# Performance work log

Hardware: AMD Instinct MI355X
Metric: run time of the kernel (lower is better)

## Reference

```python
import jax, jax.numpy as jnp
import numpy as np

DIM = 1024
INTER = 1408
N_EXPERTS = 16
TOPK = 2
N_SHARED = 2
SHARED_INTER = N_SHARED * INTER
ROUTE_SCALE = 1.0


def setup_inputs() -> dict:
    key = jax.random.key(0)
    ks = jax.random.split(key, 16)
    s = 0.02
    return {
        "x": jax.random.normal(ks[0], (2, 2048, DIM), dtype=jnp.float32),
        "gate_w": jax.random.normal(ks[1], (DIM, N_EXPERTS), dtype=jnp.float32) * s,
        "gate_b": jnp.zeros((N_EXPERTS,), dtype=jnp.float32),
        "w1": jax.random.normal(ks[2], (N_EXPERTS, DIM, INTER), dtype=jnp.float32) * s,
        "b1": jnp.zeros((N_EXPERTS, INTER), dtype=jnp.float32),
        "w3": jax.random.normal(ks[3], (N_EXPERTS, DIM, INTER), dtype=jnp.float32) * s,
        "b3": jnp.zeros((N_EXPERTS, INTER), dtype=jnp.float32),
        "w2": jax.random.normal(ks[4], (N_EXPERTS, INTER, DIM), dtype=jnp.float32) * s,
        "b2": jnp.zeros((N_EXPERTS, DIM), dtype=jnp.float32),
        "sw1": jax.random.normal(ks[5], (DIM, SHARED_INTER), dtype=jnp.float32) * s,
        "sb1": jax.random.normal(ks[6], (SHARED_INTER,), dtype=jnp.float32) * s,
        "sw3": jax.random.normal(ks[7], (DIM, SHARED_INTER), dtype=jnp.float32) * s,
        "sb3": jax.random.normal(ks[8], (SHARED_INTER,), dtype=jnp.float32) * s,
        "sw2": jax.random.normal(ks[9], (SHARED_INTER, DIM), dtype=jnp.float32) * s,
        "sb2": jax.random.normal(ks[10], (DIM,), dtype=jnp.float32) * s,
    }


def reference(x, gate_w, gate_b, w1, b1, w3, b3, w2, b2, sw1, sb1, sw3, sb3, sw2, sb2):
    shape = x.shape
    xf = x.reshape(-1, DIM)  # [T, D]

    # Gate: softmax scores in fp32, top-k routing
    logits = xf @ gate_w + gate_b  # [T, E]
    scores = jax.nn.softmax(logits.astype(jnp.float32), axis=-1)
    top_vals, top_idx = jax.lax.top_k(scores, TOPK)  # [T, K]
    weights = (top_vals * ROUTE_SCALE).astype(x.dtype)

    # Combine weights per expert: [T, E]; zero for unselected experts
    cw = (jax.nn.one_hot(top_idx, N_EXPERTS, dtype=x.dtype) * weights[..., None]).sum(axis=1)

    # Routed experts (dense-per-expert SwiGLU, masked by combine weights)
    h = jnp.einsum('td,edh->teh', xf, w1) + b1  # [T, E, I]
    g = jnp.einsum('td,edh->teh', xf, w3) + b3
    a = jax.nn.silu(h) * g
    y = jnp.einsum('teh,ehd,te->td', a, w2, cw) + cw @ b2  # [T, D]

    # Shared expert SwiGLU
    z = (jax.nn.silu(xf @ sw1 + sb1) * (xf @ sw3 + sb3)) @ sw2 + sb2

    return (y + z).reshape(shape)
```

## Files before the change

kernel.cpp:

```cpp
#include <hip/hip_runtime.h>
#include <cstdint>
#include <cstddef>

#define T_TOKENS 4096
#define DIM      1024
#define INTER    1408
#define NEXP     16
#define SINTER   2816

typedef uint32_t u32;
typedef uint16_t u16;

using s8v = __attribute__((ext_vector_type(8))) short;
using f4v = __attribute__((ext_vector_type(4))) float;

__device__ __forceinline__ u16 f2bf(float f) {
  u32 u = __float_as_uint(f);
  return (u16)((u + 0x7fffu + ((u >> 16) & 1u)) >> 16);
}
__device__ __forceinline__ u32 pack2(float a, float b) {
  return (u32)f2bf(a) | ((u32)f2bf(b) << 16);
}

__device__ __forceinline__ void load_lds16(const u16* g, u16* l) {
  __builtin_amdgcn_global_load_lds((const __attribute__((address_space(1))) void*)g,
                                   (__attribute__((address_space(3))) void*)l,
                                   16, 0, 0);
}

__global__ __launch_bounds__(256)
void cvt_x(const float* __restrict__ in, u16* __restrict__ out) {
  const int i = (blockIdx.x * 256 + threadIdx.x) * 8;
  float4 a = *(const float4*)(in + i);
  float4 b = *(const float4*)(in + i + 4);
  uint4 o;
  o.x = pack2(a.x, a.y); o.y = pack2(a.z, a.w);
  o.z = pack2(b.x, b.y); o.w = pack2(b.z, b.w);
  *(uint4*)(out + i) = o;
}

__global__ __launch_bounds__(256)
void transpose_cvt(const float* __restrict__ in, u16* __restrict__ out,
                   int K, int N) {
  const size_t eoff = (size_t)blockIdx.z * K * N;
  const int n0 = blockIdx.x * 64, k0 = blockIdx.y * 64;
  __shared__ u16 t[64][72];

  const int tid = threadIdx.x;
  {
    const int r = tid >> 4, c4 = (tid & 15) * 4;
    const float* src = in + eoff + (size_t)k0 * N + n0;
#pragma unroll
    for (int i = 0; i < 4; i++) {
      int row = r + i * 16;
      float4 v = *(const float4*)(src + (size_t)row * N + c4);
      t[c4 + 0][row] = f2bf(v.x);
      t[c4 + 1][row] = f2bf(v.y);
      t[c4 + 2][row] = f2bf(v.z);
      t[c4 + 3][row] = f2bf(v.w);
    }
  }
  __syncthreads();
  {
    const int r = tid >> 3, cc = (tid & 7) * 8;
    u16* dst = out + eoff + (size_t)n0 * K + k0;
#pragma unroll
    for (int i = 0; i < 2; i++) {
      int row = r + i * 32;
      uint4 v = *(const uint4*)&t[row][cc];
      *(uint4*)(dst + (size_t)row * K + cc) = v;
    }
  }
}

__global__ __launch_bounds__(256)
void gate_kernel(const float* __restrict__ x, const float* __restrict__ gw,
                 const float* __restrict__ gb, int* __restrict__ counts,
                 int* __restrict__ g_e, int* __restrict__ g_r, float* __restrict__ g_w)
{
  const int tok  = blockIdx.x * 4 + (threadIdx.x >> 6);
  const int lane = threadIdx.x & 63;
  const float* xr = x + (size_t)tok * DIM;

  float acc[NEXP];
#pragma unroll
  for (int e = 0; e < NEXP; e++) acc[e] = 0.f;

  for (int k = lane; k < DIM; k += 64) {
    float xv = xr[k];
    const float* gwr = gw + k * NEXP;
#pragma unroll
    for (int e = 0; e < NEXP; e++) acc[e] = fmaf(xv, gwr[e], acc[e]);
  }
#pragma unroll
  for (int e = 0; e < NEXP; e++) {
    float v = acc[e];
#pragma unroll
    for (int off = 32; off > 0; off >>= 1) v += __shfl_xor(v, off, 64);
    acc[e] = v + gb[e];
  }
  if (lane == 0) {
    float mx = acc[0];
#pragma unroll
    for (int e = 1; e < NEXP; e++) mx = fmaxf(mx, acc[e]);
    float p[NEXP]; float s = 0.f;
#pragma unroll
    for (int e = 0; e < NEXP; e++) { p[e] = expf(acc[e] - mx); s += p[e]; }
    float inv = 1.f / s;
    int i0 = -1, i1 = -1; float v0 = -1e30f, v1 = -1e30f;
#pragma unroll
    for (int e = 0; e < NEXP; e++) {
      float pe = p[e] * inv;
      if (pe > v0)      { v1 = v0; i1 = i0; v0 = pe; i0 = e; }
      else if (pe > v1) { v1 = pe; i1 = e; }
    }
    int r0 = atomicAdd(&counts[i0], 1);
    int r1 = atomicAdd(&counts[i1], 1);
    g_e[tok * 2 + 0] = i0;  g_e[tok * 2 + 1] = i1;
    g_r[tok * 2 + 0] = r0;  g_r[tok * 2 + 1] = r1;
    g_w[tok * 2 + 0] = v0;  g_w[tok * 2 + 1] = v1;
  }
}

__global__ void scan_kernel(const int* __restrict__ counts, int* __restrict__ offsets) {
  if (threadIdx.x == 0) {
    int s = 0;
#pragma unroll
    for (int e = 0; e < NEXP; e++) { offsets[e] = s; s += counts[e]; }
    offsets[NEXP] = s;
  }
}

__global__ __launch_bounds__(256)
void scatter_kernel(const int* __restrict__ g_e, const int* __restrict__ g_r,
                    const float* __restrict__ g_w, const int* __restrict__ offsets,
                    int* __restrict__ tok_slot, float* __restrict__ w_slot)
{
  int t = blockIdx.x * blockDim.x + threadIdx.x;
  if (t >= T_TOKENS) return;
#pragma unroll
  for (int k = 0; k < 2; k++) {
    int e = g_e[t * 2 + k];
    int slot = offsets[e] + g_r[t * 2 + k];
    tok_slot[slot] = t;
    w_slot[slot] = g_w[t * 2 + k];
  }
}

template<bool GATHER>
__global__ __launch_bounds__(256, 2)
void ffn_up2(const u16* __restrict__ xbf,
             const u16* __restrict__ w1t, const float* __restrict__ b1p,
             const u16* __restrict__ w3t, const float* __restrict__ b3p,
             int N,
             const int* __restrict__ offsets, const int* __restrict__ tok_slot,
             u16* __restrict__ act)
{
  int e = 0, rowbase = 0, count = T_TOKENS;
  if constexpr (GATHER) {
    e = blockIdx.z; rowbase = offsets[e]; count = offsets[e + 1] - rowbase;
  }
  const int m0 = blockIdx.y * 128;
  if (m0 >= count) return;
  const int n0 = blockIdx.x * 128;

  const u16* W1 = w1t + (size_t)e * N * DIM;
  const u16* W3 = w3t + (size_t)e * N * DIM;
  const float* B1 = b1p + (size_t)e * N;
  const float* B3 = b3p + (size_t)e * N;

  __shared__ u16 sA[128 * 32];
  __shared__ u16 sB1[128 * 32];
  __shared__ u16 sB3[128 * 32];

  const int tid = threadIdx.x;
  const int lane = tid & 63;
  const int w = tid >> 6;

  const int kc8 = (lane & 3) * 8;
  const u16* aptr[2]; const u16* b1ptr[2]; const u16* b3ptr[2];
  u16 *ldsA[2], *ldsB1[2], *ldsB3[2];
#pragma unroll
  for (int i = 0; i < 2; i++) {
    const int row = i * 64 + w * 16 + (lane >> 2);
    const int ldoff = i * 2048 + w * 512 + lane * 8;
    ldsA[i] = sA + ldoff; ldsB1[i] = sB1 + ldoff; ldsB3[i] = sB3 + ldoff;
    int arow = m0 + row; if (arow > count - 1) arow = count - 1;
    const int tok = GATHER ? tok_slot[rowbase + arow] : arow;
    aptr[i]  = xbf + (size_t)tok * DIM + kc8;
    const int brow = n0 + row;
    b1ptr[i] = W1 + (size_t)brow * DIM + kc8;
    b3ptr[i] = W3 + (size_t)brow * DIM + kc8;
  }

  const int ln = lane & 15, q = lane >> 4;
  const int wm = (w & 1) * 64, wn = (w >> 1) * 64;
  const u16* pa  = sA  + (wm + ln) * 32 + q * 8;
  const u16* pb1 = sB1 + (wn + ln) * 32 + q * 8;
  const u16* pb3 = sB3 + (wn + ln) * 32 + q * 8;

  f4v acc1[4][4] = {};
  f4v acc3[4][4] = {};

  for (int k0 = 0; k0 < DIM; k0 += 32) {
    __syncthreads();
#pragma unroll
    for (int i = 0; i < 2; i++) {
      load_lds16(aptr[i]  + k0, ldsA[i]);
      load_lds16(b1ptr[i] + k0, ldsB1[i]);
      load_lds16(b3ptr[i] + k0, ldsB3[i]);
    }
    __syncthreads();

    s8v af[4];
#pragma unroll
    for (int i = 0; i < 4; i++) af[i] = *(const s8v*)(pa + i * 512);
#pragma unroll
    for (int j = 0; j < 4; j++) {
      s8v bf1 = *(const s8v*)(pb1 + j * 512);
#pragma unroll
      for (int i = 0; i < 4; i++)
        acc1[i][j] = __builtin_amdgcn_mfma_f32_16x16x32_bf16(af[i], bf1, acc1[i][j], 0, 0, 0);
      s8v bf3 = *(const s8v*)(pb3 + j * 512);
#pragma unroll
      for (int i = 0; i < 4; i++)
        acc3[i][j] = __builtin_amdgcn_mfma_f32_16x16x32_bf16(af[i], bf3, acc3[i][j], 0, 0, 0);
    }
  }

  float bb1[4], bb3[4];
#pragma unroll
  for (int j = 0; j < 4; j++) {
    const int col = n0 + wn + j * 16 + ln;
    bb1[j] = B1[col]; bb3[j] = B3[col];
  }
#pragma unroll
  for (int i = 0; i < 4; i++) {
#pragma unroll
    for (int r = 0; r < 4; r++) {
      const int row = m0 + wm + i * 16 + q * 4 + r;
      if (row >= count) continue;
      u16* ap = act + (size_t)(rowbase + row) * N + n0 + wn;
#pragma unroll
      for (int j = 0; j < 4; j++) {
        float h = acc1[i][j][r] + bb1[j];
        float g = acc3[i][j][r] + bb3[j];
        float sv = 1.f / (1.f + __expf(-h));
        ap[j * 16 + ln] = f2bf(h * sv * g);
      }
    }
  }
}

template<bool SCATTER>
__global__ __launch_bounds__(256, 2)
void ffn_down2(const u16* __restrict__ act, int KA,
               const u16* __restrict__ w2t, const float* __restrict__ b2p,
               const int* __restrict__ offsets, const int* __restrict__ tok_slot,
               const float* __restrict__ w_slot, float* __restrict__ out)
{
  int e = 0, rowbase = 0, count = T_TOKENS;
  if constexpr (SCATTER) {
    e = blockIdx.z; rowbase = offsets[e]; count = offsets[e + 1] - rowbase;
  }
  const int m0 = blockIdx.y * 128;
  if (m0 >= count) return;
  const int n0 = blockIdx.x * 128;

  const u16* W2 = w2t + (size_t)e * DIM * KA;
  const float* B2 = b2p + (size_t)e * DIM;

  __shared__ u16 sA[128 * 32];
  __shared__ u16 sB[128 * 32];

  const int tid = threadIdx.x;
  const int lane = tid & 63;
  const int w = tid >> 6;

  const int kc8 = (lane & 3) * 8;
  const u16* aptr[2]; const u16* bptr[2];
  u16 *ldsA[2], *ldsB[2];
#pragma unroll
  for (int i = 0; i < 2; i++) {
    const int row = i * 64 + w * 16 + (lane >> 2);
    const int ldoff = i * 2048 + w * 512 + lane * 8;
    ldsA[i] = sA + ldoff; ldsB[i] = sB + ldoff;
    int arow = m0 + row; if (arow > count - 1) arow = count - 1;
    aptr[i] = act + (size_t)(rowbase + arow) * KA + kc8;
    bptr[i] = W2 + (size_t)(n0 + row) * KA + kc8;
  }

  const int ln = lane & 15, q = lane >> 4;
  const int wm = (w & 1) * 64, wn = (w >> 1) * 64;
  const u16* pa = sA + (wm + ln) * 32 + q * 8;
  const u16* pb = sB + (wn + ln) * 32 + q * 8;

  f4v acc[4][4] = {};

  for (int k0 = 0; k0 < KA; k0 += 32) {
    __syncthreads();
#pragma unroll
    for (int i = 0; i < 2; i++) {
      load_lds16(aptr[i] + k0, ldsA[i]);
      load_lds16(bptr[i] + k0, ldsB[i]);
    }
    __syncthreads();

    s8v af[4];
#pragma unroll
    for (int i = 0; i < 4; i++) af[i] = *(const s8v*)(pa + i * 512);
#pragma unroll
    for (int j = 0; j < 4; j++) {
      s8v bf = *(const s8v*)(pb + j * 512);
#pragma unroll
      for (int i = 0; i < 4; i++)
        acc[i][j] = __builtin_amdgcn_mfma_f32_16x16x32_bf16(af[i], bf, acc[i][j], 0, 0, 0);
    }
  }

  float bb[4];
#pragma unroll
  for (int j = 0; j < 4; j++) bb[j] = B2[n0 + wn + j * 16 + ln];

#pragma unroll
  for (int i = 0; i < 4; i++) {
#pragma unroll
    for (int r = 0; r < 4; r++) {
      const int row = m0 + wm + i * 16 + q * 4 + r;
      if (row >= count) continue;
      if constexpr (SCATTER) {
        const int slot = rowbase + row;
        const int tok = tok_slot[slot];
        const float wgt = w_slot[slot];
        float* orow = out + (size_t)tok * DIM + n0 + wn;
#pragma unroll
        for (int j = 0; j < 4; j++)
          atomicAdd(&orow[j * 16 + ln], wgt * (acc[i][j][r] + bb[j]));
      } else {
        float* orow = out + (size_t)row * DIM + n0 + wn;
#pragma unroll
        for (int j = 0; j < 4; j++)
          orow[j * 16 + ln] = acc[i][j][r] + bb[j];
      }
    }
  }
}

extern "C" void kernel_launch(void* const* d_in, const int* in_sizes, int n_in,
                              void* d_out, int out_size, void* d_ws, size_t ws_size,
                              hipStream_t stream)
{
  const float* x   = (const float*)d_in[0];
  const float* gw  = (const float*)d_in[1];
  const float* gb  = (const float*)d_in[2];
  const float* w1  = (const float*)d_in[3];
  const float* b1  = (const float*)d_in[4];
  const float* w3  = (const float*)d_in[5];
  const float* b3  = (const float*)d_in[6];
  const float* w2  = (const float*)d_in[7];
  const float* b2  = (const float*)d_in[8];
  const float* sw1 = (const float*)d_in[9];
  const float* sb1 = (const float*)d_in[10];
  const float* sw3 = (const float*)d_in[11];
  const float* sb3 = (const float*)d_in[12];
  const float* sw2 = (const float*)d_in[13];
  const float* sb2 = (const float*)d_in[14];
  float* out = (float*)d_out;

  char* ws = (char*)d_ws;
  size_t off = 0;
  auto alloc = [&](size_t bytes) -> char* {
    off = (off + 255) & ~(size_t)255;
    char* p = ws + off;
    off += bytes;
    return p;
  };
  int*   counts   = (int*)  alloc(NEXP * 4);
  int*   offsets  = (int*)  alloc((NEXP + 1) * 4);
  int*   g_e      = (int*)  alloc((size_t)T_TOKENS * 2 * 4);
  int*   g_r      = (int*)  alloc((size_t)T_TOKENS * 2 * 4);
  float* g_w      = (float*)alloc((size_t)T_TOKENS * 2 * 4);
  int*   tok_slot = (int*)  alloc((size_t)T_TOKENS * 2 * 4);
  float* w_slot   = (float*)alloc((size_t)T_TOKENS * 2 * 4);
  u16*   xbf      = (u16*)  alloc((size_t)T_TOKENS * DIM * 2);
  u16*   w1t      = (u16*)  alloc((size_t)NEXP * INTER * DIM * 2);
  u16*   w3t      = (u16*)  alloc((size_t)NEXP * INTER * DIM * 2);
  u16*   w2t      = (u16*)  alloc((size_t)NEXP * DIM * INTER * 2);
  u16*   sw1t     = (u16*)  alloc((size_t)SINTER * DIM * 2);
  u16*   sw3t     = (u16*)  alloc((size_t)SINTER * DIM * 2);
  u16*   sw2t     = (u16*)  alloc((size_t)DIM * SINTER * 2);
  u16*   A_act    = (u16*)  alloc((size_t)T_TOKENS * 2 * INTER * 2);
  u16*   S_act    = (u16*)  alloc((size_t)T_TOKENS * SINTER * 2);
  (void)ws_size; (void)in_sizes; (void)n_in; (void)out_size;

  hipMemsetAsync(counts, 0, NEXP * 4, stream);

  cvt_x<<<(T_TOKENS * DIM) / (256 * 8), 256, 0, stream>>>(x, xbf);
  transpose_cvt<<<dim3(INTER / 64, DIM / 64, NEXP), 256, 0, stream>>>(w1, w1t, DIM, INTER);
  transpose_cvt<<<dim3(INTER / 64, DIM / 64, NEXP), 256, 0, stream>>>(w3, w3t, DIM, INTER);
  transpose_cvt<<<dim3(DIM / 64, INTER / 64, NEXP), 256, 0, stream>>>(w2, w2t, INTER, DIM);
  transpose_cvt<<<dim3(SINTER / 64, DIM / 64, 1), 256, 0, stream>>>(sw1, sw1t, DIM, SINTER);
  transpose_cvt<<<dim3(SINTER / 64, DIM / 64, 1), 256, 0, stream>>>(sw3, sw3t, DIM, SINTER);
  transpose_cvt<<<dim3(DIM / 64, SINTER / 64, 1), 256, 0, stream>>>(sw2, sw2t, SINTER, DIM);

  gate_kernel<<<T_TOKENS / 4, 256, 0, stream>>>(x, gw, gb, counts, g_e, g_r, g_w);
  scan_kernel<<<1, 64, 0, stream>>>(counts, offsets);
  scatter_kernel<<<T_TOKENS / 256, 256, 0, stream>>>(g_e, g_r, g_w, offsets, tok_slot, w_slot);

  ffn_up2<false><<<dim3(SINTER / 128, T_TOKENS / 128, 1), 256, 0, stream>>>(
      xbf, sw1t, sb1, sw3t, sb3, SINTER, nullptr, nullptr, S_act);
  ffn_down2<false><<<dim3(DIM / 128, T_TOKENS / 128, 1), 256, 0, stream>>>(
      S_act, SINTER, sw2t, sb2, nullptr, nullptr, nullptr, out);

  ffn_up2<true><<<dim3(INTER / 128, T_TOKENS / 128, NEXP), 256, 0, stream>>>(
      xbf, w1t, b1, w3t, b3, INTER, offsets, tok_slot, A_act);
  ffn_down2<true><<<dim3(DIM / 128, T_TOKENS / 128, NEXP), 256, 0, stream>>>(
      A_act, INTER, w2t, b2, offsets, tok_slot, w_slot, out);
}
```

Measured before the change: 776.8 us.

## Replace atomic gate routing with deterministic single-block histogram route build

The gate kernel now has each lane compute one expert logit over a strided quarter of DIM, then does softmax and top-2 with wave shuffles instead of serial per-lane work. The atomic counters, memset, scan and scatter kernels are replaced by one single-block kernel that builds per-thread histograms, prefix-sums them and scatters tokens in deterministic order. This cuts launches and atomics, and ordering tokens by index within each expert may improve gather locality. The cost is a serial single-block routing step, and __expf may differ slightly from expf.

New measurement: 693.4 us. 1.12x faster.

```diff
diff --git a/kernel.cpp b/kernel.cpp
--- a/kernel.cpp
+++ b/kernel.cpp
@@ -74,76 +74,92 @@
 }
 
 __global__ __launch_bounds__(256)
-void gate_kernel(const float* __restrict__ x, const float* __restrict__ gw,
-                 const float* __restrict__ gb, int* __restrict__ counts,
-                 int* __restrict__ g_e, int* __restrict__ g_r, float* __restrict__ g_w)
+void gate_logits(const float* __restrict__ x, const float* __restrict__ gw,
+                 const float* __restrict__ gb,
+                 int* __restrict__ g_e, float* __restrict__ g_w)
 {
   const int tok  = blockIdx.x * 4 + (threadIdx.x >> 6);
   const int lane = threadIdx.x & 63;
+  const int e = lane & 15, s = lane >> 4;
   const float* xr = x + (size_t)tok * DIM;
 
-  float acc[NEXP];
-#pragma unroll
-  for (int e = 0; e < NEXP; e++) acc[e] = 0.f;
-
-  for (int k = lane; k < DIM; k += 64) {
-    float xv = xr[k];
-    const float* gwr = gw + k * NEXP;
-#pragma unroll
-    for (int e = 0; e < NEXP; e++) acc[e] = fmaf(xv, gwr[e], acc[e]);
-  }
-#pragma unroll
-  for (int e = 0; e < NEXP; e++) {
-    float v = acc[e];
-#pragma unroll
-    for (int off = 32; off > 0; off >>= 1) v += __shfl_xor(v, off, 64);
-    acc[e] = v + gb[e];
+  float acc = 0.f;
+#pragma unroll 8
+  for (int i = 0; i < DIM / 4; i++) {
+    const int k = i * 4 + s;
+    acc = fmaf(xr[k], gw[i * 64 + lane], acc);
+  }
+  acc += __shfl_xor(acc, 16, 64);
+  acc += __shfl_xor(acc, 32, 64);
+  const float logit = acc + gb[e];
+
+  float mx = logit;
+#pragma unroll
+  for (int o = 1; o < 16; o <<= 1) mx = fmaxf(mx, __shfl_xor(mx, o, 64));
+  float p = __expf(logit - mx);
+  float sum = p;
+#pragma unroll
+  for (int o = 1; o < 16; o <<= 1) sum += __shfl_xor(sum, o, 64);
+  p /= sum;
+
+  float m0 = p; int i0 = e;
+#pragma unroll
+  for (int o = 1; o < 16; o <<= 1) {
+    float om = __shfl_xor(m0, o, 64); int oi = __shfl_xor(i0, o, 64);
+    if (om > m0 || (om == m0 && oi < i0)) { m0 = om; i0 = oi; }
+  }
+  float p1 = (e == i0) ? -1.f : p;
+  float m1 = p1; int i1 = e;
+#pragma unroll
+  for (int o = 1; o < 16; o <<= 1) {
+    float om = __shfl_xor(m1, o, 64); int oi = __shfl_xor(i1, o, 64);
+    if (om > m1 || (om == m1 && oi < i1)) { m1 = om; i1 = oi; }
   }
   if (lane == 0) {
-    float mx = acc[0];
-#pragma unroll
-    for (int e = 1; e < NEXP; e++) mx = fmaxf(mx, acc[e]);
-    float p[NEXP]; float s = 0.f;
-#pragma unroll
-    for (int e = 0; e < NEXP; e++) { p[e] = expf(acc[e] - mx); s += p[e]; }
-    float inv = 1.f / s;
-    int i0 = -1, i1 = -1; float v0 = -1e30f, v1 = -1e30f;
-#pragma unroll
-    for (int e = 0; e < NEXP; e++) {
-      float pe = p[e] * inv;
-      if (pe > v0)      { v1 = v0; i1 = i0; v0 = pe; i0 = e; }
-      else if (pe > v1) { v1 = pe; i1 = e; }
-    }
-    int r0 = atomicAdd(&counts[i0], 1);
-    int r1 = atomicAdd(&counts[i1], 1);
     g_e[tok * 2 + 0] = i0;  g_e[tok * 2 + 1] = i1;
-    g_r[tok * 2 + 0] = r0;  g_r[tok * 2 + 1] = r1;
-    g_w[tok * 2 + 0] = v0;  g_w[tok * 2 + 1] = v1;
-  }
-}
-
-__global__ void scan_kernel(const int* __restrict__ counts, int* __restrict__ offsets) {
-  if (threadIdx.x == 0) {
-    int s = 0;
-#pragma unroll
-    for (int e = 0; e < NEXP; e++) { offsets[e] = s; s += counts[e]; }
-    offsets[NEXP] = s;
+    g_w[tok * 2 + 0] = m0;  g_w[tok * 2 + 1] = m1;
   }
 }
 
 __global__ __launch_bounds__(256)
-void scatter_kernel(const int* __restrict__ g_e, const int* __restrict__ g_r,
-                    const float* __restrict__ g_w, const int* __restrict__ offsets,
-                    int* __restrict__ tok_slot, float* __restrict__ w_slot)
+void route_build(const int* __restrict__ g_e, const float* __restrict__ g_w,
+                 int* __restrict__ offsets,
+                 int* __restrict__ tok_slot, float* __restrict__ w_slot)
 {
-  int t = blockIdx.x * blockDim.x + threadIdx.x;
-  if (t >= T_TOKENS) return;
-#pragma unroll
-  for (int k = 0; k < 2; k++) {
-    int e = g_e[t * 2 + k];
-    int slot = offsets[e] + g_r[t * 2 + k];
-    tok_slot[slot] = t;
-    w_slot[slot] = g_w[t * 2 + k];
+  __shared__ int hist[256][NEXP + 1];
+  __shared__ int base[NEXP + 1];
+  const int tid = threadIdx.x;
+  const int TPT = T_TOKENS / 256;
+  const int t0 = tid * TPT;
+
+#pragma unroll
+  for (int e = 0; e < NEXP; e++) hist[tid][e] = 0;
+  for (int t = t0; t < t0 + TPT; t++) {
+    hist[tid][g_e[t * 2 + 0]]++;
+    hist[tid][g_e[t * 2 + 1]]++;
+  }
+  __syncthreads();
+  if (tid < NEXP) {
+    int run = 0;
+    for (int i = 0; i < 256; i++) { int v = hist[i][tid]; hist[i][tid] = run; run += v; }
+    base[tid] = run;
+  }
+  __syncthreads();
+  if (tid == 0) {
+    int run = 0;
+#pragma unroll
+    for (int e = 0; e < NEXP; e++) { int c = base[e]; base[e] = run; offsets[e] = run; run += c; }
+    base[NEXP] = run; offsets[NEXP] = run;
+  }
+  __syncthreads();
+  for (int t = t0; t < t0 + TPT; t++) {
+#pragma unroll
+    for (int k = 0; k < 2; k++) {
+      const int e = g_e[t * 2 + k];
+      const int slot = base[e] + hist[tid][e]++;
+      tok_slot[slot] = t;
+      w_slot[slot] = g_w[t * 2 + k];
+    }
   }
 }
 
@@ -375,10 +391,8 @@
     off += bytes;
     return p;
   };
-  int*   counts   = (int*)  alloc(NEXP * 4);
   int*   offsets  = (int*)  alloc((NEXP + 1) * 4);
   int*   g_e      = (int*)  alloc((size_t)T_TOKENS * 2 * 4);
-  int*   g_r      = (int*)  alloc((size_t)T_TOKENS * 2 * 4);
   float* g_w      = (float*)alloc((size_t)T_TOKENS * 2 * 4);
   int*   tok_slot = (int*)  alloc((size_t)T_TOKENS * 2 * 4);
   float* w_slot   = (float*)alloc((size_t)T_TOKENS * 2 * 4);
@@ -393,7 +407,8 @@
   u16*   S_act    = (u16*)  alloc((size_t)T_TOKENS * SINTER * 2);
   (void)ws_size; (void)in_sizes; (void)n_in; (void)out_size;
 
-  hipMemsetAsync(counts, 0, NEXP * 4, stream);
+  gate_logits<<<T_TOKENS / 4, 256, 0, stream>>>(x, gw, gb, g_e, g_w);
+  route_build<<<1, 256, 0, stream>>>(g_e, g_w, offsets, tok_slot, w_slot);
 
   cvt_x<<<(T_TOKENS * DIM) / (256 * 8), 256, 0, stream>>>(x, xbf);
   transpose_cvt<<<dim3(INTER / 64, DIM / 64, NEXP), 256, 0, stream>>>(w1, w1t, DIM, INTER);
@@ -403,10 +418,6 @@
   transpose_cvt<<<dim3(SINTER / 64, DIM / 64, 1), 256, 0, stream>>>(sw3, sw3t, DIM, SINTER);
   transpose_cvt<<<dim3(DIM / 64, SINTER / 64, 1), 256, 0, stream>>>(sw2, sw2t, SINTER, DIM);
 
-  gate_kernel<<<T_TOKENS / 4, 256, 0, stream>>>(x, gw, gb, counts, g_e, g_r, g_w);
-  scan_kernel<<<1, 64, 0, stream>>>(counts, offsets);
-  scatter_kernel<<<T_TOKENS / 256, 256, 0, stream>>>(g_e, g_r, g_w, offsets, tok_slot, w_slot);
-
   ffn_up2<false><<<dim3(SINTER / 128, T_TOKENS / 128, 1), 256, 0, stream>>>(
       xbf, sw1t, sb1, sw3t, sb3, SINTER, nullptr, nullptr, S_act);
   ffn_down2<false><<<dim3(DIM / 128, T_TOKENS / 128, 1), 256, 0, stream>>>(
```
